# Optimization experiments

Hardware: AMD Instinct MI355X
Metric: run time of the kernel (lower is better)

Reference implementation:

```python
import math
import jax, jax.numpy as jnp
import numpy as np

D_MODEL = 1024
NUM_HEADS = 16
D_K = D_MODEL // NUM_HEADS
THETA = 10000.0
MAX_SEQ_LEN = 2048
BATCH = 2
SEQ = 2048


def build_rope_matrices(theta, d_k, max_seq_len):
    # Faithful to the torch buffer: per-position d_k x d_k tridiagonal rotation matrix.
    k = jnp.arange(d_k)
    inv_freq = jnp.power(theta, -2.0 * (k // 2) / d_k)  # [d_k]
    pos = jnp.arange(max_seq_len, dtype=jnp.float32)[:, None]  # [S,1]
    ang = pos * inv_freq[None, :]  # [S, d_k]
    cos_v = jnp.cos(ang)  # main diagonal
    sin_v = jnp.sin(jnp.where(k % 2 == 0, ang, 0.0))[:, :-1]  # sub/super diagonal, len d_k-1

    def mk(c, s):
        return jnp.diag(c) + jnp.diag(s, -1) + jnp.diag(-s, 1)

    return jax.vmap(mk)(cos_v, sin_v)  # [max_seq_len, d_k, d_k]


def setup_inputs() -> dict:
    key = jax.random.key(0)
    k1, k2, k3 = jax.random.split(key, 3)
    x = jax.random.normal(k1, (BATCH, SEQ, D_MODEL), dtype=jnp.float32)
    token_positions = jnp.arange(SEQ, dtype=jnp.int64 if jax.config.jax_enable_x64 else jnp.int32)
    # trunc_normal init approximated by scaled normal (same distribution family / scale)
    std_attn = 2.0 / (D_MODEL + 3 * D_MODEL)
    std_out = 2.0 / (D_MODEL + D_MODEL)
    W_attn = jax.random.normal(k2, (3 * NUM_HEADS * D_K, D_MODEL), dtype=jnp.float32) * std_attn
    W_out = jax.random.normal(k3, (D_MODEL, NUM_HEADS * D_K), dtype=jnp.float32) * std_out
    rope = build_rope_matrices(THETA, D_K, MAX_SEQ_LEN)
    return {"x": x, "W_attn": W_attn, "W_out": W_out, "rope": rope,
            "token_positions": token_positions}


def reference(x, W_attn, W_out, rope, token_positions):
    B, S, _ = x.shape
    # QKV projection: '... d_in, d_out d_in -> ... d_out'
    proj = jnp.einsum('bsd,ed->bse', x, W_attn)  # [B,S,3*H*dk]
    proj = proj.reshape(B, S, 3, NUM_HEADS, D_K)
    proj = jnp.transpose(proj, (2, 0, 3, 1, 4))  # [3,B,H,S,dk]
    Q, K, V = proj[0], proj[1], proj[2]
    # RoPE via per-position matrix multiply (faithful to module)
    R = rope[token_positions]  # [S, dk, dk]
    Q = jnp.einsum('sij,bhsj->bhsi', R, Q)
    K = jnp.einsum('sij,bhsj->bhsi', R, K)
    # naive causal attention with full score matrix (faithful)
    scores = jnp.einsum('bhnd,bhmd->bhnm', Q, K) / math.sqrt(D_K)
    causal = jnp.tril(jnp.ones((S, S), dtype=bool))
    scores = jnp.where(causal, scores, -jnp.inf)
    attn = jax.nn.softmax(scores, axis=-1)
    attended = jnp.einsum('bhnm,bhmd->bhnd', attn, V)  # [B,H,S,dk]
    concat = jnp.transpose(attended, (0, 2, 1, 3)).reshape(B, S, NUM_HEADS * D_K)
    return jnp.einsum('bse,de->bsd', concat, W_out)
```

## Files before the change

### kernel.cpp

```cpp
#include <hip/hip_runtime.h>
#include <math.h>

#define B_SZ 2
#define SEQ 2048
#define DMODEL 1024
#define NH 16
#define DK 64
#define NQKV 3072
#define M_ROWS 4096

#define NEG_BIG (-3.0e38f)

typedef short short8 __attribute__((ext_vector_type(8)));
typedef float v4f __attribute__((ext_vector_type(4)));
typedef unsigned short ushort_t;

__device__ inline ushort_t f2bf(float f) {
    unsigned u = __float_as_uint(f);
    u += 0x7fffu + ((u >> 16) & 1u);
    return (ushort_t)(u >> 16);
}

__device__ __forceinline__ void gl_lds16(const ushort_t* g, ushort_t* l) {
    __builtin_amdgcn_global_load_lds(
        (const __attribute__((address_space(1))) unsigned int*)g,
        (__attribute__((address_space(3))) unsigned int*)l, 16, 0, 0);
}

__global__ __launch_bounds__(256) void prep_kernel(
    const float* __restrict__ x, const float* __restrict__ Wa,
    const float* __restrict__ Wo, const float* __restrict__ rope,
    ushort_t* __restrict__ xb, ushort_t* __restrict__ Wab, ushort_t* __restrict__ Wob,
    float* __restrict__ cosT, float* __restrict__ sinT)
{
    const int bid = blockIdx.x;
    if (bid < 8192) {
        const float* src; ushort_t* dst; int i;
        if (bid < 4096)      { src = x;  dst = xb;  i = bid * 256 + threadIdx.x; }
        else if (bid < 7168) { src = Wa; dst = Wab; i = (bid - 4096) * 256 + threadIdx.x; }
        else                 { src = Wo; dst = Wob; i = (bid - 7168) * 256 + threadIdx.x; }
        float4 v = reinterpret_cast<const float4*>(src)[i];
        ushort4 r;
        r.x = f2bf(v.x); r.y = f2bf(v.y); r.z = f2bf(v.z); r.w = f2bf(v.w);
        reinterpret_cast<ushort4*>(dst)[i] = r;
    } else {
        const int i = (bid - 8192) * 256 + threadIdx.x;
        const int p = i >> 6, d = i & 63;
        const float* Rp = rope + (size_t)p * 4096;
        const float c = Rp[d * 64 + d];
        const float s = Rp[(d | 1) * 64 + (d & ~1)];
        cosT[i] = c;
        sinT[i] = (d & 1) ? s : -s;
    }
}

#define ES_STRIDE 136
extern __shared__ ushort_t qkv_smem[];

__global__ __launch_bounds__(256) void qkv_mfma_kernel(
    const ushort_t* __restrict__ xb,
    const ushort_t* __restrict__ Wab,
    const float* __restrict__ cosT, const float* __restrict__ sinT,
    const int* __restrict__ tpos,
    ushort_t* __restrict__ Qb, ushort_t* __restrict__ Kb, ushort_t* __restrict__ Vb)
{
    ushort_t* Es = qkv_smem;

    const int tid = threadIdx.x;
    const int w = tid >> 6, lane = tid & 63;
    const int lm = lane & 15, g = lane >> 4, lk8 = g * 8;
    const int wm = (w >> 1) * 64, wn = (w & 1) * 64;
    const int e0 = blockIdx.x * 128, m0 = blockIdx.y * 128;

    int srow[8], skc[8];
#pragma unroll
    for (int j = 0; j < 8; ++j) {
        const int c = tid + 256 * j;
        const int cm = c & 1023;
        const int row = cm >> 3, pp = cm & 7;
        srow[j] = row;
        skc[j] = (pp ^ (row & 7)) * 8;
    }

    v4f acc[4][4] = {};

    for (int k0 = 0; k0 < DMODEL; k0 += 64) {
        __syncthreads();
#pragma unroll
        for (int j = 0; j < 4; ++j)
            gl_lds16(&Wab[(size_t)(e0 + srow[j]) * DMODEL + k0 + skc[j]],
                     &qkv_smem[(tid + 256 * j) * 8]);
#pragma unroll
        for (int j = 4; j < 8; ++j)
            gl_lds16(&xb [(size_t)(m0 + srow[j]) * DMODEL + k0 + skc[j]],
                     &qkv_smem[(tid + 256 * j) * 8]);
        __syncthreads();

#pragma unroll
        for (int kb = 0; kb < 2; ++kb) {
            short8 af[4], bfr[4];
#pragma unroll
            for (int mf = 0; mf < 4; ++mf) {
                const int r = wm + mf * 16 + lm;
                af[mf] = *reinterpret_cast<const short8*>(
                    &qkv_smem[(r * 8 + ((kb * 4 + g) ^ (r & 7))) * 8]);
            }
#pragma unroll
            for (int nf = 0; nf < 4; ++nf) {
                const int r = wn + nf * 16 + lm;
                bfr[nf] = *reinterpret_cast<const short8*>(
                    &qkv_smem[8192 + (r * 8 + ((kb * 4 + g) ^ (r & 7))) * 8]);
            }
#pragma unroll
            for (int mf = 0; mf < 4; ++mf)
#pragma unroll
                for (int nf = 0; nf < 4; ++nf)
                    acc[mf][nf] = __builtin_amdgcn_mfma_f32_16x16x32_bf16(af[mf], bfr[nf], acc[mf][nf], 0, 0, 0);
        }
    }

    __syncthreads();

    const int which = e0 >> 10;
    ushort_t* buf = (which == 0) ? Qb : ((which == 1) ? Kb : Vb);
    const int h0 = (e0 & 1023) >> 6;
    const int bb = m0 >> 11, s0 = m0 & 2047;

#pragma unroll
    for (int mf = 0; mf < 4; ++mf) {
        const int ebase = wm + mf * 16 + g * 4;
        const int d0 = (e0 + ebase) & 63;
#pragma unroll
        for (int nf = 0; nf < 4; ++nf) {
            const int sloc = wn + nf * 16 + lm;
            float v[4] = {acc[mf][nf][0], acc[mf][nf][1], acc[mf][nf][2], acc[mf][nf][3]};
            if (which < 2) {
                const int p = tpos[s0 + sloc];
                const float4 c4 = *reinterpret_cast<const float4*>(&cosT[p * 64 + d0]);
                const float4 s4 = *reinterpret_cast<const float4*>(&sinT[p * 64 + d0]);
                const float r0 = c4.x * v[0] + s4.x * v[1];
                const float r1 = c4.y * v[1] + s4.y * v[0];
                const float r2 = c4.z * v[2] + s4.z * v[3];
                const float r3 = c4.w * v[3] + s4.w * v[2];
                v[0] = r0; v[1] = r1; v[2] = r2; v[3] = r3;
            }
            uint2 pp;
            pp.x = (unsigned)f2bf(v[0]) | ((unsigned)f2bf(v[1]) << 16);
            pp.y = (unsigned)f2bf(v[2]) | ((unsigned)f2bf(v[3]) << 16);
            *reinterpret_cast<uint2*>(&Es[sloc * ES_STRIDE + ebase]) = pp;
        }
    }
    __syncthreads();

#pragma unroll
    for (int hh = 0; hh < 2; ++hh) {
        ushort_t* dst = buf + (((size_t)bb * NH + h0 + hh) * SEQ + s0) * DK;
#pragma unroll
        for (int t = 0; t < 4; ++t) {
            const int o = (t * 256 + tid) * 8;
            const int sloc = o >> 6, d = o & 63;
            const short8 vv = *reinterpret_cast<const short8*>(&Es[sloc * ES_STRIDE + hh * 64 + d]);
            *reinterpret_cast<short8*>(&dst[o]) = vv;
        }
    }
}

__global__ __launch_bounds__(256) void transpose_v_kernel(
    const ushort_t* __restrict__ Vb, ushort_t* __restrict__ Vtb)
{
    __shared__ ushort_t t[64][72];
    const int tid = threadIdx.x;
    const int s0 = blockIdx.x * 64;
    const int hb = blockIdx.y;
    const size_t base = (size_t)hb * SEQ * DK;
#pragma unroll
    for (int r = 0; r < 2; ++r) {
        const int c = tid + 256 * r;
        const int row = c >> 3, col8 = (c & 7) * 8;
        short8 v = *reinterpret_cast<const short8*>(&Vb[base + (size_t)(s0 + row) * DK + col8]);
#pragma unroll
        for (int j = 0; j < 8; ++j) t[col8 + j][row] = (ushort_t)v[j];
    }
    __syncthreads();
#pragma unroll
    for (int r = 0; r < 2; ++r) {
        const int c = tid + 256 * r;
        const int drow = c >> 3, s8 = (c & 7) * 8;
        short8 v = *reinterpret_cast<const short8*>(&t[drow][s8]);
        *reinterpret_cast<short8*>(&Vtb[base + (size_t)drow * SEQ + s0 + s8]) = v;
    }
}

#define ATTN_STEP(QF0, QF1, QROW, LSUM, OA, DIAG, C0)                             \
    {                                                                             \
        v4f sacc[4] = {};                                                         \
        _Pragma("unroll")                                                         \
        for (int nf = 0; nf < 4; ++nf) {                                          \
            const short8 kf0 = *reinterpret_cast<const short8*>(&Ks[nf * 16 + lm][lk8]);       \
            const short8 kf1 = *reinterpret_cast<const short8*>(&Ks[nf * 16 + lm][32 + lk8]);  \
            sacc[nf] = __builtin_amdgcn_mfma_f32_16x16x32_bf16(kf0, QF0, sacc[nf], 0, 0, 0);   \
            sacc[nf] = __builtin_amdgcn_mfma_f32_16x16x32_bf16(kf1, QF1, sacc[nf], 0, 0, 0);   \
        }                                                                         \
        if (DIAG) {                                                               \
            _Pragma("unroll")                                                     \
            for (int nf = 0; nf < 4; ++nf)                                        \
                _Pragma("unroll")                                                 \
                for (int reg = 0; reg < 4; ++reg) {                               \
                    const int kv = (C0) + nf * 16 + g * 4 + reg;                  \
                    const float sv = sacc[nf][reg] * 0.125f;                      \
                    sacc[nf][reg] = (kv > (QROW)) ? NEG_BIG : sv;                 \
                }                                                                 \
        } else {                                                                  \
            _Pragma("unroll")                                                     \
            for (int nf = 0; nf < 4; ++nf)                                        \
                _Pragma("unroll")                                                 \
                for (int reg = 0; reg < 4; ++reg) sacc[nf][reg] *= 0.125f;        \
        }                                                                         \
        _Pragma("unroll")                                                         \
        for (int nf = 0; nf < 4; ++nf) {                                          \
            _Pragma("unroll")                                                     \
            for (int reg = 0; reg < 4; ++reg) {                                   \
                const float p = __expf(sacc[nf][reg]);                            \
                sacc[nf][reg] = p;                                                \
                LSUM += p;                                                        \
            }                                                                     \
            uint2 pp;                                                             \
            pp.x = (unsigned)f2bf(sacc[nf][0]) | ((unsigned)f2bf(sacc[nf][1]) << 16); \
            pp.y = (unsigned)f2bf(sacc[nf][2]) | ((unsigned)f2bf(sacc[nf][3]) << 16); \
            *reinterpret_cast<uint2*>(&Ps[w * 16 + lm][nf * 16 + g * 4]) = pp;    \
        }                                                                         \
        _Pragma("unroll")                                                         \
        for (int kc = 0; kc < 2; ++kc) {                                          \
            const short8 pf = *reinterpret_cast<const short8*>(&Ps[w * 16 + lm][kc * 32 + lk8]); \
            _Pragma("unroll")                                                     \
            for (int df = 0; df < 4; ++df) {                                      \
                const short8 vf = *reinterpret_cast<const short8*>(&Vs[df * 16 + lm][kc * 32 + lk8]); \
                OA[df] = __builtin_amdgcn_mfma_f32_16x16x32_bf16(vf, pf, OA[df], 0, 0, 0); \
            }                                                                     \
        }                                                                         \
    }

__global__ __launch_bounds__(256) void attn_mfma_kernel(
    const ushort_t* __restrict__ Qb, const ushort_t* __restrict__ Kb,
    const ushort_t* __restrict__ Vtb, ushort_t* __restrict__ attb)
{
    __shared__ ushort_t Ks[64][72];
    __shared__ ushort_t Vs[64][72];
    __shared__ ushort_t Ps[64][72];

    const int tid = threadIdx.x;
    const int w = tid >> 6, lane = tid & 63;
    const int lm = lane & 15, g = lane >> 4, lk8 = g * 8;

    const int u = blockIdx.x;
    const int h = blockIdx.y, b = blockIdx.z;
    const size_t ho = ((size_t)b * NH + h) * SEQ * DK;
    const ushort_t* Qh = Qb + ho;
    const ushort_t* Kh = Kb + ho;
    const ushort_t* Vth = Vtb + ho;

    const int rr0 = tid >> 3, cc80 = (tid & 7) * 8;
    const int rr1 = (tid + 256) >> 3, cc81 = ((tid + 256) & 7) * 8;

    const int it1 = u, it2 = 31 - u;
    const int qrowA = it1 * 64 + w * 16 + lm;
    const int qrowB = it2 * 64 + w * 16 + lm;

    const short8 qa0 = *reinterpret_cast<const short8*>(&Qh[(size_t)qrowA * DK + lk8]);
    const short8 qa1 = *reinterpret_cast<const short8*>(&Qh[(size_t)qrowA * DK + 32 + lk8]);
    const short8 qb0 = *reinterpret_cast<const short8*>(&Qh[(size_t)qrowB * DK + lk8]);
    const short8 qb1 = *reinterpret_cast<const short8*>(&Qh[(size_t)qrowB * DK + 32 + lk8]);

    float lA = 0.f, lB = 0.f;
    v4f OA[4] = {}, OB[4] = {};

    short8 kreg[2], vreg[2];
    kreg[0] = *reinterpret_cast<const short8*>(&Kh[(size_t)rr0 * DK + cc80]);
    kreg[1] = *reinterpret_cast<const short8*>(&Kh[(size_t)rr1 * DK + cc81]);
    vreg[0] = *reinterpret_cast<const short8*>(&Vth[(size_t)rr0 * SEQ + cc80]);
    vreg[1] = *reinterpret_cast<const short8*>(&Vth[(size_t)rr1 * SEQ + cc81]);

    for (int jt = 0; jt <= it2; ++jt) {
        const int c0 = jt * 64;

        __syncthreads();
        *reinterpret_cast<short8*>(&Ks[rr0][cc80]) = kreg[0];
        *reinterpret_cast<short8*>(&Ks[rr1][cc81]) = kreg[1];
        *reinterpret_cast<short8*>(&Vs[rr0][cc80]) = vreg[0];
        *reinterpret_cast<short8*>(&Vs[rr1][cc81]) = vreg[1];
        __syncthreads();

        if (jt < it2) {
            const int c0n = c0 + 64;
            kreg[0] = *reinterpret_cast<const short8*>(&Kh[(size_t)(c0n + rr0) * DK + cc80]);
            kreg[1] = *reinterpret_cast<const short8*>(&Kh[(size_t)(c0n + rr1) * DK + cc81]);
            vreg[0] = *reinterpret_cast<const short8*>(&Vth[(size_t)rr0 * SEQ + c0n + cc80]);
            vreg[1] = *reinterpret_cast<const short8*>(&Vth[(size_t)rr1 * SEQ + c0n + cc81]);
        }

        ATTN_STEP(qb0, qb1, qrowB, lB, OB, (jt == it2), c0)
        if (jt <= it1) {
            ATTN_STEP(qa0, qa1, qrowA, lA, OA, (jt == it1), c0)
        }
    }

    lA += __shfl_xor(lA, 16, 64); lA += __shfl_xor(lA, 32, 64);
    lB += __shfl_xor(lB, 16, 64); lB += __shfl_xor(lB, 32, 64);
    {
        const float inv = 1.0f / lA;
#pragma unroll
        for (int df = 0; df < 4; ++df) {
            const unsigned lo = (unsigned)f2bf(OA[df][0] * inv) | ((unsigned)f2bf(OA[df][1] * inv) << 16);
            const unsigned hi = (unsigned)f2bf(OA[df][2] * inv) | ((unsigned)f2bf(OA[df][3] * inv) << 16);
            uint2 st; st.x = lo; st.y = hi;
            *reinterpret_cast<uint2*>(
                &attb[((size_t)b * SEQ + qrowA) * DMODEL + h * DK + df * 16 + g * 4]) = st;
        }
    }
    {
        const float inv = 1.0f / lB;
#pragma unroll
        for (int df = 0; df < 4; ++df) {
            const unsigned lo = (unsigned)f2bf(OB[df][0] * inv) | ((unsigned)f2bf(OB[df][1] * inv) << 16);
            const unsigned hi = (unsigned)f2bf(OB[df][2] * inv) | ((unsigned)f2bf(OB[df][3] * inv) << 16);
            uint2 st; st.x = lo; st.y = hi;
            *reinterpret_cast<uint2*>(
                &attb[((size_t)b * SEQ + qrowB) * DMODEL + h * DK + df * 16 + g * 4]) = st;
        }
    }
}

__global__ __launch_bounds__(256) void out_mfma_kernel(
    const ushort_t* __restrict__ attb,
    const ushort_t* __restrict__ Wob,
    float* __restrict__ out)
{
    __shared__ ushort_t smem[16384];

    const int tid = threadIdx.x;
    const int w = tid >> 6, lane = tid & 63;
    const int lm = lane & 15, g = lane >> 4;
    const int wm = (w >> 1) * 64, wn = (w & 1) * 64;
    const int m0 = blockIdx.y * 128, n0 = blockIdx.x * 128;

    int srow[8], skc[8];
#pragma unroll
    for (int j = 0; j < 8; ++j) {
        const int c = tid + 256 * j;
        const int cm = c & 1023;
        const int row = cm >> 3, pp = cm & 7;
        srow[j] = row;
        skc[j] = (pp ^ (row & 7)) * 8;
    }

    v4f acc[4][4] = {};

    for (int k0 = 0; k0 < DMODEL; k0 += 64) {
        __syncthreads();
#pragma unroll
        for (int j = 0; j < 4; ++j)
            gl_lds16(&attb[(size_t)(m0 + srow[j]) * DMODEL + k0 + skc[j]],
                     &smem[(tid + 256 * j) * 8]);
#pragma unroll
        for (int j = 4; j < 8; ++j)
            gl_lds16(&Wob[(size_t)(n0 + srow[j]) * DMODEL + k0 + skc[j]],
                     &smem[(tid + 256 * j) * 8]);
        __syncthreads();

#pragma unroll
        for (int kb = 0; kb < 2; ++kb) {
            short8 af[4], bfr[4];
#pragma unroll
            for (int mf = 0; mf < 4; ++mf) {
                const int r = wm + mf * 16 + lm;
                af[mf] = *reinterpret_cast<const short8*>(
                    &smem[(r * 8 + ((kb * 4 + g) ^ (r & 7))) * 8]);
            }
#pragma unroll
            for (int nf = 0; nf < 4; ++nf) {
                const int r = wn + nf * 16 + lm;
                bfr[nf] = *reinterpret_cast<const short8*>(
                    &smem[8192 + (r * 8 + ((kb * 4 + g) ^ (r & 7))) * 8]);
            }
#pragma unroll
            for (int mf = 0; mf < 4; ++mf)
#pragma unroll
                for (int nf = 0; nf < 4; ++nf)
                    acc[mf][nf] = __builtin_amdgcn_mfma_f32_16x16x32_bf16(af[mf], bfr[nf], acc[mf][nf], 0, 0, 0);
        }
    }

#pragma unroll
    for (int mf = 0; mf < 4; ++mf)
#pragma unroll
        for (int reg = 0; reg < 4; ++reg) {
            const int m = m0 + wm + mf * 16 + g * 4 + reg;
#pragma unroll
            for (int nf = 0; nf < 4; ++nf) {
                const int n = n0 + wn + nf * 16 + lm;
                out[(size_t)m * DMODEL + n] = acc[mf][nf][reg];
            }
        }
}

extern "C" void kernel_launch(void* const* d_in, const int* in_sizes, int n_in,
                              void* d_out, int out_size, void* d_ws, size_t ws_size,
                              hipStream_t stream) {
    (void)in_sizes; (void)n_in; (void)out_size; (void)ws_size;

    const float* x    = (const float*)d_in[0];
    const float* Wa   = (const float*)d_in[1];
    const float* Wo   = (const float*)d_in[2];
    const float* rope = (const float*)d_in[3];
    const int*   tp   = (const int*)d_in[4];
    float* out = (float*)d_out;

    char* ws = (char*)d_ws;
    ushort_t* xb   = (ushort_t*)(ws);
    ushort_t* Wab  = (ushort_t*)(ws + (8u << 20));
    ushort_t* Wob  = (ushort_t*)(ws + (14u << 20));
    float*    cosT = (float*)   (ws + (16u << 20));
    float*    sinT = (float*)   (ws + (16u << 20) + (512u << 10));
    ushort_t* Qb   = (ushort_t*)(ws + (17u << 20));
    ushort_t* Kb   = (ushort_t*)(ws + (25u << 20));
    ushort_t* Vb   = (ushort_t*)(ws + (33u << 20));
    ushort_t* Vtb  = (ushort_t*)(ws + (41u << 20));
    ushort_t* attb = (ushort_t*)(ws + (49u << 20));

    dim3 blk(256);
    prep_kernel<<<dim3(8704), blk, 0, stream>>>(x, Wa, Wo, rope, xb, Wab, Wob, cosT, sinT);

    const size_t qkv_lds = 128 * ES_STRIDE * sizeof(ushort_t);
    qkv_mfma_kernel<<<dim3(NQKV / 128, M_ROWS / 128), blk, qkv_lds, stream>>>(
        xb, Wab, cosT, sinT, tp, Qb, Kb, Vb);
    transpose_v_kernel<<<dim3(SEQ / 64, B_SZ * NH), blk, 0, stream>>>(Vb, Vtb);
    attn_mfma_kernel<<<dim3(16, NH, B_SZ), blk, 0, stream>>>(Qb, Kb, Vtb, attb);
    out_mfma_kernel<<<dim3(DMODEL / 128, M_ROWS / 128), blk, 0, stream>>>(attb, Wob, out);
}
```

Baseline: 230.6 us.

## Fuse V transpose into QKV epilogue, double-buffer attention K/V tiles, use exp2

The QKV GEMM epilogue now writes V directly in transposed [d, seq] layout through LDS, which removes the separate transpose kernel and its extra global round trip. The attention kernel double-buffers the K/V shared-memory tiles so each loop iteration needs one barrier instead of two. The softmax folds log2(e) into the score scale and uses exp2f. The transposed V epilogue does scalar 2-byte LDS writes, which may cause bank conflicts, and the double buffers raise LDS use in the attention kernel.

```diff
diff --git a/kernel.cpp b/kernel.cpp
--- a/kernel.cpp
+++ b/kernel.cpp
@@ -10,6 +10,7 @@
 #define M_ROWS 4096
 
 #define NEG_BIG (-3.0e38f)
+#define SCL 0.18033688011112042f
 
 typedef short short8 __attribute__((ext_vector_type(8)));
 typedef float v4f __attribute__((ext_vector_type(4)));
@@ -62,13 +63,13 @@
     const ushort_t* __restrict__ Wab,
     const float* __restrict__ cosT, const float* __restrict__ sinT,
     const int* __restrict__ tpos,
-    ushort_t* __restrict__ Qb, ushort_t* __restrict__ Kb, ushort_t* __restrict__ Vb)
+    ushort_t* __restrict__ Qb, ushort_t* __restrict__ Kb, ushort_t* __restrict__ Vtb)
 {
     ushort_t* Es = qkv_smem;
 
     const int tid = threadIdx.x;
     const int w = tid >> 6, lane = tid & 63;
-    const int lm = lane & 15, g = lane >> 4, lk8 = g * 8;
+    const int lm = lane & 15, g = lane >> 4;
     const int wm = (w >> 1) * 64, wn = (w & 1) * 64;
     const int e0 = blockIdx.x * 128, m0 = blockIdx.y * 128;
 
@@ -122,19 +123,19 @@
     __syncthreads();
 
     const int which = e0 >> 10;
-    ushort_t* buf = (which == 0) ? Qb : ((which == 1) ? Kb : Vb);
     const int h0 = (e0 & 1023) >> 6;
     const int bb = m0 >> 11, s0 = m0 & 2047;
 
-#pragma unroll
-    for (int mf = 0; mf < 4; ++mf) {
-        const int ebase = wm + mf * 16 + g * 4;
-        const int d0 = (e0 + ebase) & 63;
-#pragma unroll
-        for (int nf = 0; nf < 4; ++nf) {
-            const int sloc = wn + nf * 16 + lm;
-            float v[4] = {acc[mf][nf][0], acc[mf][nf][1], acc[mf][nf][2], acc[mf][nf][3]};
-            if (which < 2) {
+    if (which < 2) {
+        ushort_t* buf = (which == 0) ? Qb : Kb;
+#pragma unroll
+        for (int mf = 0; mf < 4; ++mf) {
+            const int ebase = wm + mf * 16 + g * 4;
+            const int d0 = (e0 + ebase) & 63;
+#pragma unroll
+            for (int nf = 0; nf < 4; ++nf) {
+                const int sloc = wn + nf * 16 + lm;
+                float v[4] = {acc[mf][nf][0], acc[mf][nf][1], acc[mf][nf][2], acc[mf][nf][3]};
                 const int p = tpos[s0 + sloc];
                 const float4 c4 = *reinterpret_cast<const float4*>(&cosT[p * 64 + d0]);
                 const float4 s4 = *reinterpret_cast<const float4*>(&sinT[p * 64 + d0]);
@@ -142,62 +143,57 @@
                 const float r1 = c4.y * v[1] + s4.y * v[0];
                 const float r2 = c4.z * v[2] + s4.z * v[3];
                 const float r3 = c4.w * v[3] + s4.w * v[2];
-                v[0] = r0; v[1] = r1; v[2] = r2; v[3] = r3;
-            }
-            uint2 pp;
-            pp.x = (unsigned)f2bf(v[0]) | ((unsigned)f2bf(v[1]) << 16);
-            pp.y = (unsigned)f2bf(v[2]) | ((unsigned)f2bf(v[3]) << 16);
-            *reinterpret_cast<uint2*>(&Es[sloc * ES_STRIDE + ebase]) = pp;
-        }
-    }
-    __syncthreads();
-
-#pragma unroll
-    for (int hh = 0; hh < 2; ++hh) {
-        ushort_t* dst = buf + (((size_t)bb * NH + h0 + hh) * SEQ + s0) * DK;
-#pragma unroll
-        for (int t = 0; t < 4; ++t) {
-            const int o = (t * 256 + tid) * 8;
-            const int sloc = o >> 6, d = o & 63;
-            const short8 vv = *reinterpret_cast<const short8*>(&Es[sloc * ES_STRIDE + hh * 64 + d]);
-            *reinterpret_cast<short8*>(&dst[o]) = vv;
-        }
-    }
-}
-
-__global__ __launch_bounds__(256) void transpose_v_kernel(
-    const ushort_t* __restrict__ Vb, ushort_t* __restrict__ Vtb)
-{
-    __shared__ ushort_t t[64][72];
-    const int tid = threadIdx.x;
-    const int s0 = blockIdx.x * 64;
-    const int hb = blockIdx.y;
-    const size_t base = (size_t)hb * SEQ * DK;
-#pragma unroll
-    for (int r = 0; r < 2; ++r) {
-        const int c = tid + 256 * r;
-        const int row = c >> 3, col8 = (c & 7) * 8;
-        short8 v = *reinterpret_cast<const short8*>(&Vb[base + (size_t)(s0 + row) * DK + col8]);
-#pragma unroll
-        for (int j = 0; j < 8; ++j) t[col8 + j][row] = (ushort_t)v[j];
-    }
-    __syncthreads();
-#pragma unroll
-    for (int r = 0; r < 2; ++r) {
-        const int c = tid + 256 * r;
-        const int drow = c >> 3, s8 = (c & 7) * 8;
-        short8 v = *reinterpret_cast<const short8*>(&t[drow][s8]);
-        *reinterpret_cast<short8*>(&Vtb[base + (size_t)drow * SEQ + s0 + s8]) = v;
-    }
-}
-
-#define ATTN_STEP(QF0, QF1, QROW, LSUM, OA, DIAG, C0)                             \
+                uint2 pp;
+                pp.x = (unsigned)f2bf(r0) | ((unsigned)f2bf(r1) << 16);
+                pp.y = (unsigned)f2bf(r2) | ((unsigned)f2bf(r3) << 16);
+                *reinterpret_cast<uint2*>(&Es[sloc * ES_STRIDE + ebase]) = pp;
+            }
+        }
+        __syncthreads();
+#pragma unroll
+        for (int hh = 0; hh < 2; ++hh) {
+            ushort_t* dst = buf + (((size_t)bb * NH + h0 + hh) * SEQ + s0) * DK;
+#pragma unroll
+            for (int t = 0; t < 4; ++t) {
+                const int o = (t * 256 + tid) * 8;
+                const int sloc = o >> 6, d = o & 63;
+                const short8 vv = *reinterpret_cast<const short8*>(&Es[sloc * ES_STRIDE + hh * 64 + d]);
+                *reinterpret_cast<short8*>(&dst[o]) = vv;
+            }
+        }
+    } else {
+#pragma unroll
+        for (int mf = 0; mf < 4; ++mf) {
+            const int ebase = wm + mf * 16 + g * 4;
+#pragma unroll
+            for (int nf = 0; nf < 4; ++nf) {
+                const int sloc = wn + nf * 16 + lm;
+                Es[(ebase + 0) * ES_STRIDE + sloc] = f2bf(acc[mf][nf][0]);
+                Es[(ebase + 1) * ES_STRIDE + sloc] = f2bf(acc[mf][nf][1]);
+                Es[(ebase + 2) * ES_STRIDE + sloc] = f2bf(acc[mf][nf][2]);
+                Es[(ebase + 3) * ES_STRIDE + sloc] = f2bf(acc[mf][nf][3]);
+            }
+        }
+        __syncthreads();
+#pragma unroll
+        for (int t = 0; t < 8; ++t) {
+            const int c = t * 256 + tid;
+            const int hh = c >> 10, cm = c & 1023;
+            const int d = cm >> 4, s8c = (cm & 15) * 8;
+            const short8 vv = *reinterpret_cast<const short8*>(&Es[(hh * 64 + d) * ES_STRIDE + s8c]);
+            ushort_t* dst = Vtb + ((size_t)bb * NH + h0 + hh) * SEQ * DK + (size_t)d * SEQ + s0 + s8c;
+            *reinterpret_cast<short8*>(dst) = vv;
+        }
+    }
+}
+
+#define ATTN_STEP(KSB, VSB, QF0, QF1, QROW, LSUM, OA, DIAG, C0)                   \
     {                                                                             \
         v4f sacc[4] = {};                                                         \
         _Pragma("unroll")                                                         \
         for (int nf = 0; nf < 4; ++nf) {                                          \
-            const short8 kf0 = *reinterpret_cast<const short8*>(&Ks[nf * 16 + lm][lk8]);       \
-            const short8 kf1 = *reinterpret_cast<const short8*>(&Ks[nf * 16 + lm][32 + lk8]);  \
+            const short8 kf0 = *reinterpret_cast<const short8*>(&KSB[nf * 16 + lm][lk8]);      \
+            const short8 kf1 = *reinterpret_cast<const short8*>(&KSB[nf * 16 + lm][32 + lk8]); \
             sacc[nf] = __builtin_amdgcn_mfma_f32_16x16x32_bf16(kf0, QF0, sacc[nf], 0, 0, 0);   \
             sacc[nf] = __builtin_amdgcn_mfma_f32_16x16x32_bf16(kf1, QF1, sacc[nf], 0, 0, 0);   \
         }                                                                         \
@@ -207,20 +203,20 @@
                 _Pragma("unroll")                                                 \
                 for (int reg = 0; reg < 4; ++reg) {                               \
                     const int kv = (C0) + nf * 16 + g * 4 + reg;                  \
-                    const float sv = sacc[nf][reg] * 0.125f;                      \
+                    const float sv = sacc[nf][reg] * SCL;                         \
                     sacc[nf][reg] = (kv > (QROW)) ? NEG_BIG : sv;                 \
                 }                                                                 \
         } else {                                                                  \
             _Pragma("unroll")                                                     \
             for (int nf = 0; nf < 4; ++nf)                                        \
                 _Pragma("unroll")                                                 \
-                for (int reg = 0; reg < 4; ++reg) sacc[nf][reg] *= 0.125f;        \
+                for (int reg = 0; reg < 4; ++reg) sacc[nf][reg] *= SCL;           \
         }                                                                         \
         _Pragma("unroll")                                                         \
         for (int nf = 0; nf < 4; ++nf) {                                          \
             _Pragma("unroll")                                                     \
             for (int reg = 0; reg < 4; ++reg) {                                   \
-                const float p = __expf(sacc[nf][reg]);                            \
+                const float p = exp2f(sacc[nf][reg]);                             \
                 sacc[nf][reg] = p;                                                \
                 LSUM += p;                                                        \
             }                                                                     \
@@ -234,7 +230,7 @@
             const short8 pf = *reinterpret_cast<const short8*>(&Ps[w * 16 + lm][kc * 32 + lk8]); \
             _Pragma("unroll")                                                     \
             for (int df = 0; df < 4; ++df) {                                      \
-                const short8 vf = *reinterpret_cast<const short8*>(&Vs[df * 16 + lm][kc * 32 + lk8]); \
+                const short8 vf = *reinterpret_cast<const short8*>(&VSB[df * 16 + lm][kc * 32 + lk8]); \
                 OA[df] = __builtin_amdgcn_mfma_f32_16x16x32_bf16(vf, pf, OA[df], 0, 0, 0); \
             }                                                                     \
         }                                                                         \
@@ -244,8 +240,8 @@
     const ushort_t* __restrict__ Qb, const ushort_t* __restrict__ Kb,
     const ushort_t* __restrict__ Vtb, ushort_t* __restrict__ attb)
 {
-    __shared__ ushort_t Ks[64][72];
-    __shared__ ushort_t Vs[64][72];
+    __shared__ ushort_t Ks[2][64][72];
+    __shared__ ushort_t Vs[2][64][72];
     __shared__ ushort_t Ps[64][72];
 
     const int tid = threadIdx.x;
@@ -282,13 +278,14 @@
 
     for (int jt = 0; jt <= it2; ++jt) {
         const int c0 = jt * 64;
-
-        __syncthreads();
-        *reinterpret_cast<short8*>(&Ks[rr0][cc80]) = kreg[0];
-        *reinterpret_cast<short8*>(&Ks[rr1][cc81]) = kreg[1];
-        *reinterpret_cast<short8*>(&Vs[rr0][cc80]) = vreg[0];
-        *reinterpret_cast<short8*>(&Vs[rr1][cc81]) = vreg[1];
-        __syncthreads();
+        const int bufi = jt & 1;
+        ushort_t (*Ksb)[72] = Ks[bufi];
+        ushort_t (*Vsb)[72] = Vs[bufi];
+
+        *reinterpret_cast<short8*>(&Ksb[rr0][cc80]) = kreg[0];
+        *reinterpret_cast<short8*>(&Ksb[rr1][cc81]) = kreg[1];
+        *reinterpret_cast<short8*>(&Vsb[rr0][cc80]) = vreg[0];
+        *reinterpret_cast<short8*>(&Vsb[rr1][cc81]) = vreg[1];
 
         if (jt < it2) {
             const int c0n = c0 + 64;
@@ -298,9 +295,11 @@
             vreg[1] = *reinterpret_cast<const short8*>(&Vth[(size_t)rr1 * SEQ + c0n + cc81]);
         }
 
-        ATTN_STEP(qb0, qb1, qrowB, lB, OB, (jt == it2), c0)
+        __syncthreads();
+
+        ATTN_STEP(Ksb, Vsb, qb0, qb1, qrowB, lB, OB, (jt == it2), c0)
         if (jt <= it1) {
-            ATTN_STEP(qa0, qa1, qrowA, lA, OA, (jt == it1), c0)
+            ATTN_STEP(Ksb, Vsb, qa0, qa1, qrowA, lA, OA, (jt == it1), c0)
         }
     }
 
@@ -423,17 +422,15 @@
     float*    sinT = (float*)   (ws + (16u << 20) + (512u << 10));
     ushort_t* Qb   = (ushort_t*)(ws + (17u << 20));
     ushort_t* Kb   = (ushort_t*)(ws + (25u << 20));
-    ushort_t* Vb   = (ushort_t*)(ws + (33u << 20));
-    ushort_t* Vtb  = (ushort_t*)(ws + (41u << 20));
-    ushort_t* attb = (ushort_t*)(ws + (49u << 20));
+    ushort_t* Vtb  = (ushort_t*)(ws + (33u << 20));
+    ushort_t* attb = (ushort_t*)(ws + (41u << 20));
 
     dim3 blk(256);
     prep_kernel<<<dim3(8704), blk, 0, stream>>>(x, Wa, Wo, rope, xb, Wab, Wob, cosT, sinT);
 
     const size_t qkv_lds = 128 * ES_STRIDE * sizeof(ushort_t);
     qkv_mfma_kernel<<<dim3(NQKV / 128, M_ROWS / 128), blk, qkv_lds, stream>>>(
-        xb, Wab, cosT, sinT, tp, Qb, Kb, Vb);
-    transpose_v_kernel<<<dim3(SEQ / 64, B_SZ * NH), blk, 0, stream>>>(Vb, Vtb);
+        xb, Wab, cosT, sinT, tp, Qb, Kb, Vtb);
     attn_mfma_kernel<<<dim3(16, NH, B_SZ), blk, 0, stream>>>(Qb, Kb, Vtb, attb);
     out_mfma_kernel<<<dim3(DMODEL / 128, M_ROWS / 128), blk, 0, stream>>>(attb, Wob, out);
 }
```

Result: no change. 226.3 us (-1.9%).
